# Optimization experiments

Hardware: AMD Instinct MI355X
Metric: run time of the kernel (lower is better)

Reference implementation:

```python
import jax, jax.numpy as jnp
import numpy as np

N = 65536          # total nodes
E = 131072         # total edges
G = 4096           # number of graphs (sessions)
NODES_PER_GRAPH = 16
H = 128            # hidden_dim
D = 64             # embedding_dim
NUM_ITEMS = 50000
NUM_CAT, NUM_SUB, NUM_EL, NUM_BR = 1000, 5000, 10000, 2000
NUM_ITERATIONS = 1


def setup_inputs() -> dict:
    key = jax.random.key(0)
    ks = jax.random.split(key, 24)
    inp = {
        "category": jax.random.randint(ks[0], (N,), 0, NUM_CAT),
        "sub_category": jax.random.randint(ks[1], (N,), 0, NUM_SUB),
        "element": jax.random.randint(ks[2], (N,), 0, NUM_EL),
        "brand": jax.random.randint(ks[3], (N,), 0, NUM_BR),
        "product_id": jax.random.randint(ks[4], (N,), 0, NUM_ITEMS),
        "price": jax.random.uniform(ks[5], (N, 1), dtype=jnp.float32),
        "edge_index": jax.random.randint(ks[6], (2, E), 0, N),
        "batch": jnp.arange(N) // NODES_PER_GRAPH,  # sorted node->graph ids
    }
    s = 0.05
    IN = 5 * D + 1  # 321
    inp["emb_cat"] = jax.random.normal(ks[7], (NUM_CAT, D), jnp.float32) * s
    inp["emb_sub"] = jax.random.normal(ks[8], (NUM_SUB, D), jnp.float32) * s
    inp["emb_el"] = jax.random.normal(ks[9], (NUM_EL, D), jnp.float32) * s
    inp["emb_br"] = jax.random.normal(ks[10], (NUM_BR, D), jnp.float32) * s
    inp["emb_item"] = jax.random.normal(ks[11], (NUM_ITEMS, D), jnp.float32) * s
    inp["Wm"] = jax.random.normal(ks[12], (H, IN), jnp.float32) * s
    inp["bm"] = jnp.zeros((H,), jnp.float32)
    inp["W_ih"] = jax.random.normal(ks[13], (3 * H, H), jnp.float32) * s
    inp["b_ih"] = jnp.zeros((3 * H,), jnp.float32)
    inp["W_hh"] = jax.random.normal(ks[14], (3 * H, H), jnp.float32) * s
    inp["b_hh"] = jnp.zeros((3 * H,), jnp.float32)
    inp["Wg1"] = jax.random.normal(ks[15], (H, H), jnp.float32) * s
    inp["bg1"] = jnp.zeros((H,), jnp.float32)
    inp["Wg2"] = jax.random.normal(ks[16], (1, H), jnp.float32) * s
    inp["bg2"] = jnp.zeros((1,), jnp.float32)
    inp["Wfc"] = jax.random.normal(ks[17], (NUM_ITEMS, H), jnp.float32) * s
    inp["bfc"] = jnp.zeros((NUM_ITEMS,), jnp.float32)
    return inp


def _forward(category, sub_category, element, brand, product_id, price,
             edge_index, batch, emb_cat, emb_sub, emb_el, emb_br, emb_item,
             Wm, bm, W_ih, b_ih, W_hh, b_hh, Wg1, bg1, Wg2, bg2, Wfc, bfc):
    # NodeEmbedding: concat of 5 lookups, then prepend price -> (N, 5D+1)
    emb = jnp.concatenate([
        emb_cat[category], emb_sub[sub_category], emb_el[element],
        emb_br[brand], emb_item[product_id]], axis=1)
    x = jnp.concatenate([price, emb], axis=1)

    # message_linear
    h = x @ Wm.T + bm  # (N, H)

    src, dst = edge_index[0], edge_index[1]  # source -> target
    for _ in range(NUM_ITERATIONS):
        # scatter-mean aggregation of source node embeddings at targets
        msg_sum = jax.ops.segment_sum(h[src], dst, num_segments=N)
        cnt = jax.ops.segment_sum(jnp.ones((E,), h.dtype), dst, num_segments=N)
        m = msg_sum / jnp.maximum(cnt, 1.0)[:, None]
        # GRUCell(m, h), PyTorch gate layout [r, z, n]
        gi = m @ W_ih.T + b_ih
        gh = h @ W_hh.T + b_hh
        gi_r, gi_z, gi_n = jnp.split(gi, 3, axis=1)
        gh_r, gh_z, gh_n = jnp.split(gh, 3, axis=1)
        r = jax.nn.sigmoid(gi_r + gh_r)
        z = jax.nn.sigmoid(gi_z + gh_z)
        n = jnp.tanh(gi_n + r * gh_n)
        h = (1.0 - z) * n + z * h

    # attentional aggregation: segment softmax over batch
    gate = (jax.nn.relu(h @ Wg1.T + bg1) @ Wg2.T + bg2)[:, 0]  # (N,)
    seg_max = jax.ops.segment_max(gate, batch, num_segments=G)
    alpha = jnp.exp(gate - seg_max[batch])
    denom = jax.ops.segment_sum(alpha, batch, num_segments=G)
    w = alpha / denom[batch]
    pooled = jax.ops.segment_sum(w[:, None] * h, batch, num_segments=G)  # (G, H)

    return pooled @ Wfc.T + bfc  # (G, num_items)


def reference(category, sub_category, element, brand, product_id, price,
              edge_index, batch, emb_cat, emb_sub, emb_el, emb_br, emb_item,
              Wm, bm, W_ih, b_ih, W_hh, b_hh, Wg1, bg1, Wg2, bg2, Wfc, bfc):
    return _forward(category, sub_category, element, brand, product_id, price,
                    edge_index, batch, emb_cat, emb_sub, emb_el, emb_br, emb_item,
                    Wm, bm, W_ih, b_ih, W_hh, b_hh, Wg1, bg1, Wg2, bg2, Wfc, bfc)
```

## Files before the change

### kernel.cpp

```cpp
#include <hip/hip_runtime.h>
#include <hip/hip_bf16.h>
#include <cstdint>
#include <cstddef>

#define NN 65536
#define EE 131072
#define GG 4096
#define HH 128
#define DD 64
#define KP 384
#define ITEMS 50000
#define NPAD 50176

typedef __attribute__((ext_vector_type(8))) short bf16x8;
typedef __attribute__((ext_vector_type(4))) float f32x4;
typedef unsigned short u16;
typedef __attribute__((ext_vector_type(4))) unsigned short u16x4;

#define PINV(x) asm volatile("" : "+v"(x))

__device__ inline void split2(float x, u16* hi, u16* lo) {
    __hip_bfloat16 h = __float2bfloat16(x);
    float hf = __bfloat162float(h);
    __hip_bfloat16 l = __float2bfloat16(x - hf);
    *hi = *reinterpret_cast<u16*>(&h);
    *lo = *reinterpret_cast<u16*>(&l);
}
__device__ inline u16 hi_only(float x) {
    __hip_bfloat16 h = __float2bfloat16(x);
    return *reinterpret_cast<u16*>(&h);
}
__device__ inline float bf2f(u16 v) {
    unsigned int u = ((unsigned int)v) << 16;
    return *reinterpret_cast<float*>(&u);
}

__global__ void k_embed(const int* __restrict__ cat, const int* __restrict__ sub,
                        const int* __restrict__ el, const int* __restrict__ br,
                        const int* __restrict__ pid, const float* __restrict__ price,
                        const float* __restrict__ ecat, const float* __restrict__ esub,
                        const float* __restrict__ eel, const float* __restrict__ ebr,
                        const float* __restrict__ eitem, u16* __restrict__ Xhi) {
    int tid = threadIdx.x;
    int n = blockIdx.x * 4 + (tid >> 6);
    int l = tid & 63;
    u16* xh = Xhi + (size_t)n * KP;
    if (l == 0) xh[0] = hi_only(price[n]);
    xh[1 + l]   = hi_only(ecat[(size_t)cat[n] * DD + l]);
    xh[65 + l]  = hi_only(esub[(size_t)sub[n] * DD + l]);
    xh[129 + l] = hi_only(eel [(size_t)el[n]  * DD + l]);
    xh[193 + l] = hi_only(ebr [(size_t)br[n]  * DD + l]);
    xh[257 + l] = hi_only(eitem[(size_t)pid[n]* DD + l]);
    if (l < 63) xh[321 + l] = 0;
}

__global__ void k_cvt_hi(const float* __restrict__ src, u16* __restrict__ hi,
                         int n_valid, int n_total) {
    int i = blockIdx.x * 256 + threadIdx.x;
    if (i >= n_total) return;
    hi[i] = (i < n_valid) ? hi_only(src[i]) : (u16)0;
}

__global__ void k_cvt_wm(const float* __restrict__ Wm, u16* __restrict__ hi) {
    int i = blockIdx.x * 256 + threadIdx.x;
    int r = i / KP, c = i - r * KP;
    float x = (c < 321) ? Wm[r * 321 + c] : 0.f;
    hi[i] = hi_only(x);
}

#define M1_STR 132
__launch_bounds__(256, 2)
__global__ void k_mlp1(const u16* __restrict__ Xhi, const u16* __restrict__ Whi,
                       const float* __restrict__ bm,
                       u16* __restrict__ hhi, u16* __restrict__ hlo) {
    __shared__ float ls[128 * M1_STR];
    int tid = threadIdx.x, w = tid >> 6, l = tid & 63;
    int lr = l & 15, lk = l >> 4;
    int m0 = blockIdx.x * 128;
    f32x4 acc[2][8];
    #pragma unroll
    for (int rt = 0; rt < 2; ++rt)
        #pragma unroll
        for (int ci = 0; ci < 8; ++ci) acc[rt][ci] = (f32x4){0.f, 0.f, 0.f, 0.f};

    for (int kc = 0; kc < 12; ++kc) {
        bf16x8 ah[2];
        #pragma unroll
        for (int rt = 0; rt < 2; ++rt) {
            size_t off = (size_t)(m0 + w * 32 + rt * 16 + lr) * KP + kc * 32 + lk * 8;
            ah[rt] = *(const bf16x8*)(Xhi + off);
        }
        #pragma unroll
        for (int ci = 0; ci < 8; ++ci) {
            size_t boff = (size_t)(ci * 16 + lr) * KP + kc * 32 + lk * 8;
            bf16x8 bh = *(const bf16x8*)(Whi + boff);
            #pragma unroll
            for (int rt = 0; rt < 2; ++rt)
                acc[rt][ci] = __builtin_amdgcn_mfma_f32_16x16x32_bf16(ah[rt], bh, acc[rt][ci], 0, 0, 0);
        }
    }
    #pragma unroll
    for (int rt = 0; rt < 2; ++rt)
        #pragma unroll
        for (int ci = 0; ci < 8; ++ci) {
            int col = ci * 16 + lr;
            float bv = bm[col];
            #pragma unroll
            for (int q = 0; q < 4; ++q)
                ls[(w * 32 + rt * 16 + lk * 4 + q) * M1_STR + col] = acc[rt][ci][q] + bv;
        }
    __syncthreads();
    int row = tid >> 1, cb = (tid & 1) * 64;
    u16* hh = hhi + (size_t)(m0 + row) * HH + cb;
    u16* hl = hlo + (size_t)(m0 + row) * HH + cb;
    #pragma unroll
    for (int i = 0; i < 64; i += 4) {
        float4 v = *(const float4*)&ls[row * M1_STR + cb + i];
        u16x4 vh, vl;
        split2(v.x, (u16*)&vh + 0, (u16*)&vl + 0);
        split2(v.y, (u16*)&vh + 1, (u16*)&vl + 1);
        split2(v.z, (u16*)&vh + 2, (u16*)&vl + 2);
        split2(v.w, (u16*)&vh + 3, (u16*)&vl + 3);
        *(u16x4*)(hh + i) = vh;
        *(u16x4*)(hl + i) = vl;
    }
}

__global__ void k_scatter(const u16* __restrict__ hhi, const int* __restrict__ edge,
                          float* __restrict__ msg, float* __restrict__ cnt) {
    int j = threadIdx.x & 127;
    int eo = threadIdx.x >> 7;
    int e0 = blockIdx.x * 16;
    #pragma unroll
    for (int it = 0; it < 8; ++it) {
        int e = e0 + it * 2 + eo;
        int s = edge[e];
        int d = edge[EE + e];
        atomicAdd(&msg[(size_t)d * HH + j], bf2f(hhi[(size_t)s * HH + j]));
        if (j == 0) atomicAdd(&cnt[d], 1.0f);
    }
}

#define GRU_STR 136
__launch_bounds__(256, 2)
__global__ void k_gru(const float* __restrict__ msg, const float* __restrict__ cnt,
                      const u16* __restrict__ Wihh, const u16* __restrict__ Whhh,
                      const float* __restrict__ b_ih, const float* __restrict__ b_hh,
                      u16* __restrict__ hhi, u16* __restrict__ hlo) {
    __shared__ float ls[32 * GRU_STR];
    int tid = threadIdx.x, w = tid >> 6, l = tid & 63;
    int lr = l & 15, lk = l >> 4;
    int m0 = blockIdx.x * 32;
    f32x4 acc[6][2][2];
    #pragma unroll
    for (int g = 0; g < 6; ++g)
        #pragma unroll
        for (int ct = 0; ct < 2; ++ct)
            #pragma unroll
            for (int rt = 0; rt < 2; ++rt) acc[g][ct][rt] = (f32x4){0.f, 0.f, 0.f, 0.f};

    float cinv[2];
    const float* mrow[2];
    #pragma unroll
    for (int rt = 0; rt < 2; ++rt) {
        int row = m0 + rt * 16 + lr;
        cinv[rt] = 1.0f / fmaxf(cnt[row], 1.0f);
        mrow[rt] = msg + (size_t)row * HH + lk * 8;
    }

    for (int kc = 0; kc < 4; ++kc) {
        bf16x8 amh[2], ahh[2];
        #pragma unroll
        for (int rt = 0; rt < 2; ++rt) {
            float4 v0 = *(const float4*)(mrow[rt] + kc * 32);
            float4 v1 = *(const float4*)(mrow[rt] + kc * 32 + 4);
            float xs[8] = {v0.x * cinv[rt], v0.y * cinv[rt], v0.z * cinv[rt], v0.w * cinv[rt],
                           v1.x * cinv[rt], v1.y * cinv[rt], v1.z * cinv[rt], v1.w * cinv[rt]};
            #pragma unroll
            for (int q = 0; q < 8; ++q) amh[rt][q] = (short)hi_only(xs[q]);
            size_t off = (size_t)(m0 + rt * 16 + lr) * HH + kc * 32 + lk * 8;
            ahh[rt] = *(const bf16x8*)(hhi + off);
        }
        #pragma unroll
        for (int g = 0; g < 6; ++g) {
            const u16* WH = (g < 3) ? Wihh : Whhh;
            int gb = (g % 3) * HH;
            #pragma unroll
            for (int ct = 0; ct < 2; ++ct) {
                size_t boff = (size_t)(gb + w * 32 + ct * 16 + lr) * HH + kc * 32 + lk * 8;
                bf16x8 bh = *(const bf16x8*)(WH + boff);
                #pragma unroll
                for (int rt = 0; rt < 2; ++rt) {
                    bf16x8 ah = (g < 3) ? amh[rt] : ahh[rt];
                    acc[g][ct][rt] = __builtin_amdgcn_mfma_f32_16x16x32_bf16(ah, bh, acc[g][ct][rt], 0, 0, 0);
                }
            }
        }
    }
    #pragma unroll
    for (int ct = 0; ct < 2; ++ct) {
        int col = w * 32 + ct * 16 + lr;
        float bir = b_ih[col], biz = b_ih[HH + col], bin = b_ih[2 * HH + col];
        float bhr = b_hh[col], bhz = b_hh[HH + col], bhn = b_hh[2 * HH + col];
        #pragma unroll
        for (int rt = 0; rt < 2; ++rt)
            #pragma unroll
            for (int q = 0; q < 4; ++q) {
                int rl = rt * 16 + lk * 4 + q;
                size_t idx = (size_t)(m0 + rl) * HH + col;
                float gir = acc[0][ct][rt][q] + bir;
                float giz = acc[1][ct][rt][q] + biz;
                float gin = acc[2][ct][rt][q] + bin;
                float ghr = acc[3][ct][rt][q] + bhr;
                float ghz = acc[4][ct][rt][q] + bhz;
                float ghn = acc[5][ct][rt][q] + bhn;
                float hv = bf2f(hhi[idx]) + bf2f(hlo[idx]);
                float r = 1.f / (1.f + expf(-(gir + ghr)));
                float z = 1.f / (1.f + expf(-(giz + ghz)));
                float nn = tanhf(gin + r * ghn);
                ls[rl * GRU_STR + col] = (1.f - z) * nn + z * hv;
            }
    }
    __syncthreads();
    int row = tid >> 3, cb = (tid & 7) * 16;
    u16* hh = hhi + (size_t)(m0 + row) * HH + cb;
    u16* hl = hlo + (size_t)(m0 + row) * HH + cb;
    #pragma unroll
    for (int i = 0; i < 16; i += 4) {
        float4 v = *(const float4*)&ls[row * GRU_STR + cb + i];
        u16x4 vh, vl;
        split2(v.x, (u16*)&vh + 0, (u16*)&vl + 0);
        split2(v.y, (u16*)&vh + 1, (u16*)&vl + 1);
        split2(v.z, (u16*)&vh + 2, (u16*)&vl + 2);
        split2(v.w, (u16*)&vh + 3, (u16*)&vl + 3);
        *(u16x4*)(hh + i) = vh;
        *(u16x4*)(hl + i) = vl;
    }
}

__launch_bounds__(256, 2)
__global__ void k_gatepool(const u16* __restrict__ hhi, const u16* __restrict__ hlo,
                           const u16* __restrict__ Ghi, const float* __restrict__ bg1,
                           const float* __restrict__ Wg2,
                           u16* __restrict__ phi, u16* __restrict__ plo) {
    __shared__ float sal[128];
    int tid = threadIdx.x, w = tid >> 6, l = tid & 63;
    int lr = l & 15, lk = l >> 4;
    int m0 = blockIdx.x * 128;
    f32x4 acc[2][8];
    #pragma unroll
    for (int rt = 0; rt < 2; ++rt)
        #pragma unroll
        for (int ci = 0; ci < 8; ++ci) acc[rt][ci] = (f32x4){0.f, 0.f, 0.f, 0.f};

    for (int kc = 0; kc < 4; ++kc) {
        bf16x8 ah[2];
        #pragma unroll
        for (int rt = 0; rt < 2; ++rt) {
            size_t off = (size_t)(m0 + w * 32 + rt * 16 + lr) * HH + kc * 32 + lk * 8;
            ah[rt] = *(const bf16x8*)(hhi + off);
        }
        #pragma unroll
        for (int ci = 0; ci < 8; ++ci) {
            size_t boff = (size_t)(ci * 16 + lr) * HH + kc * 32 + lk * 8;
            bf16x8 bh = *(const bf16x8*)(Ghi + boff);
            #pragma unroll
            for (int rt = 0; rt < 2; ++rt)
                acc[rt][ci] = __builtin_amdgcn_mfma_f32_16x16x32_bf16(ah[rt], bh, acc[rt][ci], 0, 0, 0);
        }
    }
    float part[2][4] = {};
    #pragma unroll
    for (int ci = 0; ci < 8; ++ci) {
        int col = ci * 16 + lr;
        float wv = Wg2[col], bb = bg1[col];
        #pragma unroll
        for (int rt = 0; rt < 2; ++rt)
            #pragma unroll
            for (int q = 0; q < 4; ++q)
                part[rt][q] += fmaxf(acc[rt][ci][q] + bb, 0.f) * wv;
    }
    #pragma unroll
    for (int rt = 0; rt < 2; ++rt)
        #pragma unroll
        for (int q = 0; q < 4; ++q) {
            float v = part[rt][q];
            v += __shfl_xor(v, 1);
            v += __shfl_xor(v, 2);
            v += __shfl_xor(v, 4);
            v += __shfl_xor(v, 8);
            part[rt][q] = v;
        }
    if (lr == 0) {
        #pragma unroll
        for (int rt = 0; rt < 2; ++rt)
            #pragma unroll
            for (int q = 0; q < 4; ++q)
                sal[w * 32 + rt * 16 + lk * 4 + q] = part[rt][q];
    }
    __syncthreads();

    int g2 = tid >> 5;
    int c = (tid & 31) * 4;
    int rb = g2 * 16;
    float gv[16];
    float mx = -1e30f;
    #pragma unroll
    for (int i = 0; i < 16; ++i) { gv[i] = sal[rb + i]; mx = fmaxf(mx, gv[i]); }
    float den = 0.f;
    #pragma unroll
    for (int i = 0; i < 16; ++i) { gv[i] = expf(gv[i] - mx); den += gv[i]; }
    float inv = 1.f / den;
    f32x4 a = (f32x4){0.f, 0.f, 0.f, 0.f};
    #pragma unroll
    for (int i = 0; i < 16; ++i) {
        size_t idx = (size_t)(m0 + rb + i) * HH + c;
        u16x4 xh = *(const u16x4*)(hhi + idx);
        u16x4 xl = *(const u16x4*)(hlo + idx);
        float wgt = gv[i] * inv;
        a[0] += wgt * (bf2f(xh.x) + bf2f(xl.x));
        a[1] += wgt * (bf2f(xh.y) + bf2f(xl.y));
        a[2] += wgt * (bf2f(xh.z) + bf2f(xl.z));
        a[3] += wgt * (bf2f(xh.w) + bf2f(xl.w));
    }
    size_t po = (size_t)(blockIdx.x * 8 + g2) * HH + c;
    u16x4 vh, vl;
    #pragma unroll
    for (int q = 0; q < 4; ++q) split2(a[q], (u16*)&vh + q, (u16*)&vl + q);
    *(u16x4*)(phi + po) = vh;
    *(u16x4*)(plo + po) = vl;
}

#define FC_STR 520
__launch_bounds__(256, 2)
__global__ void k_fc13(const u16* __restrict__ Wfcb,
                       const u16* __restrict__ phi, const u16* __restrict__ plo,
                       const float* __restrict__ bfc, float* __restrict__ out) {
    __shared__ float ls[2][16][FC_STR];
    int wg = blockIdx.x;
    int xcd = wg & 7;
    int r = wg >> 3;
    int strip = (r >> 2) * 8 + xcd;
    int phase = r & 3;
    if (strip >= 98) return;
    int tid = threadIdx.x, w = tid >> 6, l = tid & 63;
    int lr = l & 15, lk = l >> 4;
    int c0 = strip * 512;
    int mbase = phase * 1024;

    bf16x8 bh[8][4];
    float bias[8];
    #pragma unroll
    for (int ci = 0; ci < 8; ++ci) {
        int n = c0 + w * 128 + ci * 16 + lr;
        const u16* Wr = Wfcb + (size_t)n * HH + lk * 8;
        #pragma unroll
        for (int kc = 0; kc < 4; ++kc)
            bh[ci][kc] = *(const bf16x8*)(Wr + kc * 32);
        bias[ci] = (n < ITEMS) ? bfc[n] : 0.f;
    }
    #pragma unroll
    for (int ci = 0; ci < 8; ++ci)
        #pragma unroll
        for (int kc = 0; kc < 4; ++kc) PINV(bh[ci][kc]);

    bf16x8 a0h[4], a0l[4], a1h[4], a1l[4];
    auto LOADA = [&](int t, bf16x8* Ah, bf16x8* Al) {
        int m0 = mbase + t * 16;
        size_t aoff = (size_t)(m0 + lr) * HH + lk * 8;
        #pragma unroll
        for (int kc = 0; kc < 4; ++kc) {
            Ah[kc] = *(const bf16x8*)(phi + aoff + kc * 32);
            Al[kc] = *(const bf16x8*)(plo + aoff + kc * 32);
        }
    };
    auto COMP = [&](const bf16x8* Ah, const bf16x8* Al, int b) {
        #pragma unroll
        for (int ci = 0; ci < 8; ++ci) {
            f32x4 acc = (f32x4){0.f, 0.f, 0.f, 0.f};
            #pragma unroll
            for (int kc = 0; kc < 4; ++kc) {
                acc = __builtin_amdgcn_mfma_f32_16x16x32_bf16(Ah[kc], bh[ci][kc], acc, 0, 0, 0);
                acc = __builtin_amdgcn_mfma_f32_16x16x32_bf16(Al[kc], bh[ci][kc], acc, 0, 0, 0);
            }
            #pragma unroll
            for (int q = 0; q < 4; ++q)
                ls[b][lk * 4 + q][w * 128 + ci * 16 + lr] = acc[q] + bias[ci];
        }
    };
    auto FLUSH = [&](int t, int b) {
        int m0 = mbase + t * 16;
        #pragma unroll
        for (int p = 0; p < 4; ++p) {
            int row = w * 4 + p;
            #pragma unroll
            for (int s = 0; s < 2; ++s) {
                int c = s * 256 + l * 4;
                int gc = c0 + c;
                if (gc < ITEMS) {
                    f32x4 v = *(const f32x4*)&ls[b][row][c];
                    __builtin_nontemporal_store(v, (f32x4*)&out[(size_t)(m0 + row) * ITEMS + gc]);
                }
            }
        }
    };
    auto softbar = [&]() {
        asm volatile("s_waitcnt lgkmcnt(0)" ::: "memory");
        __builtin_amdgcn_s_barrier();
    };

    LOADA(0, a0h, a0l);
    LOADA(1, a1h, a1l);
    COMP(a0h, a0l, 0);
    softbar();
    for (int t = 1; t < 64; ++t) {
        if (t + 1 < 64) {
            if ((t + 1) & 1) LOADA(t + 1, a1h, a1l);
            else             LOADA(t + 1, a0h, a0l);
        }
        if (t & 1) COMP(a1h, a1l, 1);
        else       COMP(a0h, a0l, 0);
        FLUSH(t - 1, (t - 1) & 1);
        softbar();
    }
    FLUSH(63, 1);
}

extern "C" void kernel_launch(void* const* d_in, const int* in_sizes, int n_in,
                              void* d_out, int out_size, void* d_ws, size_t ws_size,
                              hipStream_t stream) {
    const int* category = (const int*)d_in[0];
    const int* sub_cat  = (const int*)d_in[1];
    const int* element  = (const int*)d_in[2];
    const int* brand    = (const int*)d_in[3];
    const int* pid      = (const int*)d_in[4];
    const float* price  = (const float*)d_in[5];
    const int* edge     = (const int*)d_in[6];
    const float* ecat   = (const float*)d_in[8];
    const float* esub   = (const float*)d_in[9];
    const float* eel    = (const float*)d_in[10];
    const float* ebr    = (const float*)d_in[11];
    const float* eitem  = (const float*)d_in[12];
    const float* Wm     = (const float*)d_in[13];
    const float* bm     = (const float*)d_in[14];
    const float* W_ih   = (const float*)d_in[15];
    const float* b_ih   = (const float*)d_in[16];
    const float* W_hh   = (const float*)d_in[17];
    const float* b_hh   = (const float*)d_in[18];
    const float* Wg1    = (const float*)d_in[19];
    const float* bg1    = (const float*)d_in[20];
    const float* Wg2    = (const float*)d_in[21];
    const float* Wfc    = (const float*)d_in[23];
    const float* bfc    = (const float*)d_in[24];
    float* out = (float*)d_out;

    char* p = (char*)d_ws;
    auto alloc = [&](size_t bytes) { char* r = p; p += (bytes + 255) & ~(size_t)255; return r; };
    u16* Xhi   = (u16*)alloc((size_t)NN * KP * 2);
    u16* hhi   = (u16*)alloc((size_t)NN * HH * 2);
    u16* hlo   = (u16*)alloc((size_t)NN * HH * 2);
    float* msg = (float*)alloc((size_t)NN * HH * 4);
    float* cnt = (float*)alloc((size_t)NN * 4);
    u16* phi   = (u16*)alloc((size_t)GG * HH * 2);
    u16* plo   = (u16*)alloc((size_t)GG * HH * 2);
    u16* Wmhi  = (u16*)alloc((size_t)HH * KP * 2);
    u16* Wihhi = (u16*)alloc((size_t)3 * HH * HH * 2);
    u16* Whhhi = (u16*)alloc((size_t)3 * HH * HH * 2);
    u16* Wg1hi = (u16*)alloc((size_t)HH * HH * 2);
    u16* Wfcb  = (u16*)alloc((size_t)NPAD * HH * 2);

    hipMemsetAsync(msg, 0, (size_t)NN * HH * sizeof(float), stream);
    hipMemsetAsync(cnt, 0, (size_t)NN * sizeof(float), stream);

    k_cvt_wm<<<(HH * KP + 255) / 256, 256, 0, stream>>>(Wm, Wmhi);
    k_cvt_hi<<<(3 * HH * HH + 255) / 256, 256, 0, stream>>>(W_ih, Wihhi, 3 * HH * HH, 3 * HH * HH);
    k_cvt_hi<<<(3 * HH * HH + 255) / 256, 256, 0, stream>>>(W_hh, Whhhi, 3 * HH * HH, 3 * HH * HH);
    k_cvt_hi<<<(HH * HH + 255) / 256, 256, 0, stream>>>(Wg1, Wg1hi, HH * HH, HH * HH);
    k_cvt_hi<<<(NPAD * HH + 255) / 256, 256, 0, stream>>>(Wfc, Wfcb, ITEMS * HH, NPAD * HH);

    k_embed<<<NN / 4, 256, 0, stream>>>(category, sub_cat, element, brand, pid, price,
                                        ecat, esub, eel, ebr, eitem, Xhi);
    k_mlp1<<<NN / 128, 256, 0, stream>>>(Xhi, Wmhi, bm, hhi, hlo);
    k_scatter<<<EE / 16, 256, 0, stream>>>(hhi, edge, msg, cnt);
    k_gru<<<NN / 32, 256, 0, stream>>>(msg, cnt, Wihhi, Whhhi, b_ih, b_hh, hhi, hlo);
    k_gatepool<<<NN / 128, 256, 0, stream>>>(hhi, hlo, Wg1hi, bg1, Wg2, phi, plo);
    k_fc13<<<dim3(416), 256, 0, stream>>>(Wfcb, phi, plo, bfc, out);
}
```

Before: 423.5 us.

## Accumulate messages in bf16 with packed atomics and fuse prep kernels

Replaces the fp32 message buffer with a bf16 buffer updated via packed bf16 global atomic adds, halving atomic operations and memory traffic in the scatter and GRU read. Also merges embedding gather, buffer zeroing and all weight conversions into a single prep kernel to remove launch and memset overhead. Risks accuracy loss from bf16 accumulation of summed messages.

```diff
diff --git a/kernel.cpp b/kernel.cpp
--- a/kernel.cpp
+++ b/kernel.cpp
@@ -34,38 +34,76 @@
     unsigned int u = ((unsigned int)v) << 16;
     return *reinterpret_cast<float*>(&u);
 }
-
-__global__ void k_embed(const int* __restrict__ cat, const int* __restrict__ sub,
-                        const int* __restrict__ el, const int* __restrict__ br,
-                        const int* __restrict__ pid, const float* __restrict__ price,
-                        const float* __restrict__ ecat, const float* __restrict__ esub,
-                        const float* __restrict__ eel, const float* __restrict__ ebr,
-                        const float* __restrict__ eitem, u16* __restrict__ Xhi) {
+__device__ inline void atomic_pk_bf16(u16* addr, unsigned int data) {
+    asm volatile("global_atomic_pk_add_bf16 %0, %1, off"
+                 :: "v"(addr), "v"(data) : "memory");
+}
+
+#define PREP_EMBED 16384
+#define PREP_MSGZ  4096
+#define PREP_CNTZ  64
+#define PREP_WM    192
+#define PREP_WIH   192
+#define PREP_WHH   192
+#define PREP_WG1   64
+#define PREP_WFC   25088
+__global__ void k_prep(const int* __restrict__ cat, const int* __restrict__ sub,
+                       const int* __restrict__ el, const int* __restrict__ br,
+                       const int* __restrict__ pid, const float* __restrict__ price,
+                       const float* __restrict__ ecat, const float* __restrict__ esub,
+                       const float* __restrict__ eel, const float* __restrict__ ebr,
+                       const float* __restrict__ eitem,
+                       const float* __restrict__ Wm, const float* __restrict__ W_ih,
+                       const float* __restrict__ W_hh, const float* __restrict__ Wg1,
+                       const float* __restrict__ Wfc,
+                       u16* __restrict__ Xhi, u16* __restrict__ msgb,
+                       float* __restrict__ cnt,
+                       u16* __restrict__ Wmhi, u16* __restrict__ Wihhi,
+                       u16* __restrict__ Whhhi, u16* __restrict__ Wg1hi,
+                       u16* __restrict__ Wfcb) {
+    int b = blockIdx.x;
     int tid = threadIdx.x;
-    int n = blockIdx.x * 4 + (tid >> 6);
-    int l = tid & 63;
-    u16* xh = Xhi + (size_t)n * KP;
-    if (l == 0) xh[0] = hi_only(price[n]);
-    xh[1 + l]   = hi_only(ecat[(size_t)cat[n] * DD + l]);
-    xh[65 + l]  = hi_only(esub[(size_t)sub[n] * DD + l]);
-    xh[129 + l] = hi_only(eel [(size_t)el[n]  * DD + l]);
-    xh[193 + l] = hi_only(ebr [(size_t)br[n]  * DD + l]);
-    xh[257 + l] = hi_only(eitem[(size_t)pid[n]* DD + l]);
-    if (l < 63) xh[321 + l] = 0;
-}
-
-__global__ void k_cvt_hi(const float* __restrict__ src, u16* __restrict__ hi,
-                         int n_valid, int n_total) {
-    int i = blockIdx.x * 256 + threadIdx.x;
-    if (i >= n_total) return;
-    hi[i] = (i < n_valid) ? hi_only(src[i]) : (u16)0;
-}
-
-__global__ void k_cvt_wm(const float* __restrict__ Wm, u16* __restrict__ hi) {
-    int i = blockIdx.x * 256 + threadIdx.x;
-    int r = i / KP, c = i - r * KP;
-    float x = (c < 321) ? Wm[r * 321 + c] : 0.f;
-    hi[i] = hi_only(x);
+    if (b < PREP_EMBED) {
+        int n = b * 4 + (tid >> 6);
+        int l = tid & 63;
+        u16* xh = Xhi + (size_t)n * KP;
+        if (l == 0) xh[0] = hi_only(price[n]);
+        xh[1 + l]   = hi_only(ecat[(size_t)cat[n] * DD + l]);
+        xh[65 + l]  = hi_only(esub[(size_t)sub[n] * DD + l]);
+        xh[129 + l] = hi_only(eel [(size_t)el[n]  * DD + l]);
+        xh[193 + l] = hi_only(ebr [(size_t)br[n]  * DD + l]);
+        xh[257 + l] = hi_only(eitem[(size_t)pid[n]* DD + l]);
+        if (l < 63) xh[321 + l] = 0;
+        return;
+    }
+    b -= PREP_EMBED;
+    if (b < PREP_MSGZ) {
+        ((f32x4*)msgb)[(size_t)b * 256 + tid] = (f32x4){0.f, 0.f, 0.f, 0.f};
+        return;
+    }
+    b -= PREP_MSGZ;
+    if (b < PREP_CNTZ) {
+        ((f32x4*)cnt)[(size_t)b * 256 + tid] = (f32x4){0.f, 0.f, 0.f, 0.f};
+        return;
+    }
+    b -= PREP_CNTZ;
+    if (b < PREP_WM) {
+        int i = b * 256 + tid;
+        int r = i / KP, c = i - r * KP;
+        Wmhi[i] = (c < 321) ? hi_only(Wm[r * 321 + c]) : (u16)0;
+        return;
+    }
+    b -= PREP_WM;
+    if (b < PREP_WIH) { int i = b * 256 + tid; Wihhi[i] = hi_only(W_ih[i]); return; }
+    b -= PREP_WIH;
+    if (b < PREP_WHH) { int i = b * 256 + tid; Whhhi[i] = hi_only(W_hh[i]); return; }
+    b -= PREP_WHH;
+    if (b < PREP_WG1) { int i = b * 256 + tid; Wg1hi[i] = hi_only(Wg1[i]); return; }
+    b -= PREP_WG1;
+    {
+        int i = b * 256 + tid;
+        Wfcb[i] = (i < ITEMS * HH) ? hi_only(Wfc[i]) : (u16)0;
+    }
 }
 
 #define M1_STR 132
@@ -127,23 +165,24 @@
 }
 
 __global__ void k_scatter(const u16* __restrict__ hhi, const int* __restrict__ edge,
-                          float* __restrict__ msg, float* __restrict__ cnt) {
-    int j = threadIdx.x & 127;
-    int eo = threadIdx.x >> 7;
+                          u16* __restrict__ msgb, float* __restrict__ cnt) {
+    int w = threadIdx.x >> 6;
+    int l = threadIdx.x & 63;
     int e0 = blockIdx.x * 16;
     #pragma unroll
-    for (int it = 0; it < 8; ++it) {
-        int e = e0 + it * 2 + eo;
+    for (int it = 0; it < 4; ++it) {
+        int e = e0 + it * 4 + w;
         int s = edge[e];
         int d = edge[EE + e];
-        atomicAdd(&msg[(size_t)d * HH + j], bf2f(hhi[(size_t)s * HH + j]));
-        if (j == 0) atomicAdd(&cnt[d], 1.0f);
+        unsigned int pk = *(const unsigned int*)(hhi + (size_t)s * HH + 2 * l);
+        atomic_pk_bf16(msgb + (size_t)d * HH + 2 * l, pk);
+        if (l == 0) atomicAdd(&cnt[d], 1.0f);
     }
 }
 
 #define GRU_STR 136
 __launch_bounds__(256, 2)
-__global__ void k_gru(const float* __restrict__ msg, const float* __restrict__ cnt,
+__global__ void k_gru(const u16* __restrict__ msgb, const float* __restrict__ cnt,
                       const u16* __restrict__ Wihh, const u16* __restrict__ Whhh,
                       const float* __restrict__ b_ih, const float* __restrict__ b_hh,
                       u16* __restrict__ hhi, u16* __restrict__ hlo) {
@@ -160,24 +199,22 @@
             for (int rt = 0; rt < 2; ++rt) acc[g][ct][rt] = (f32x4){0.f, 0.f, 0.f, 0.f};
 
     float cinv[2];
-    const float* mrow[2];
+    const u16* mrowb[2];
     #pragma unroll
     for (int rt = 0; rt < 2; ++rt) {
         int row = m0 + rt * 16 + lr;
         cinv[rt] = 1.0f / fmaxf(cnt[row], 1.0f);
-        mrow[rt] = msg + (size_t)row * HH + lk * 8;
+        mrowb[rt] = msgb + (size_t)row * HH + lk * 8;
     }
 
     for (int kc = 0; kc < 4; ++kc) {
         bf16x8 amh[2], ahh[2];
         #pragma unroll
         for (int rt = 0; rt < 2; ++rt) {
-            float4 v0 = *(const float4*)(mrow[rt] + kc * 32);
-            float4 v1 = *(const float4*)(mrow[rt] + kc * 32 + 4);
-            float xs[8] = {v0.x * cinv[rt], v0.y * cinv[rt], v0.z * cinv[rt], v0.w * cinv[rt],
-                           v1.x * cinv[rt], v1.y * cinv[rt], v1.z * cinv[rt], v1.w * cinv[rt]};
-            #pragma unroll
-            for (int q = 0; q < 8; ++q) amh[rt][q] = (short)hi_only(xs[q]);
+            bf16x8 mv = *(const bf16x8*)(mrowb[rt] + kc * 32);
+            #pragma unroll
+            for (int q = 0; q < 8; ++q)
+                amh[rt][q] = (short)hi_only(bf2f((u16)mv[q]) * cinv[rt]);
             size_t off = (size_t)(m0 + rt * 16 + lr) * HH + kc * 32 + lk * 8;
             ahh[rt] = *(const bf16x8*)(hhi + off);
         }
@@ -459,7 +496,7 @@
     u16* Xhi   = (u16*)alloc((size_t)NN * KP * 2);
     u16* hhi   = (u16*)alloc((size_t)NN * HH * 2);
     u16* hlo   = (u16*)alloc((size_t)NN * HH * 2);
-    float* msg = (float*)alloc((size_t)NN * HH * 4);
+    u16* msgb  = (u16*)alloc((size_t)NN * HH * 2);
     float* cnt = (float*)alloc((size_t)NN * 4);
     u16* phi   = (u16*)alloc((size_t)GG * HH * 2);
     u16* plo   = (u16*)alloc((size_t)GG * HH * 2);
@@ -469,20 +506,16 @@
     u16* Wg1hi = (u16*)alloc((size_t)HH * HH * 2);
     u16* Wfcb  = (u16*)alloc((size_t)NPAD * HH * 2);
 
-    hipMemsetAsync(msg, 0, (size_t)NN * HH * sizeof(float), stream);
-    hipMemsetAsync(cnt, 0, (size_t)NN * sizeof(float), stream);
-
-    k_cvt_wm<<<(HH * KP + 255) / 256, 256, 0, stream>>>(Wm, Wmhi);
-    k_cvt_hi<<<(3 * HH * HH + 255) / 256, 256, 0, stream>>>(W_ih, Wihhi, 3 * HH * HH, 3 * HH * HH);
-    k_cvt_hi<<<(3 * HH * HH + 255) / 256, 256, 0, stream>>>(W_hh, Whhhi, 3 * HH * HH, 3 * HH * HH);
-    k_cvt_hi<<<(HH * HH + 255) / 256, 256, 0, stream>>>(Wg1, Wg1hi, HH * HH, HH * HH);
-    k_cvt_hi<<<(NPAD * HH + 255) / 256, 256, 0, stream>>>(Wfc, Wfcb, ITEMS * HH, NPAD * HH);
-
-    k_embed<<<NN / 4, 256, 0, stream>>>(category, sub_cat, element, brand, pid, price,
-                                        ecat, esub, eel, ebr, eitem, Xhi);
+    const int prep_grid = PREP_EMBED + PREP_MSGZ + PREP_CNTZ + PREP_WM +
+                          PREP_WIH + PREP_WHH + PREP_WG1 + PREP_WFC;
+    k_prep<<<prep_grid, 256, 0, stream>>>(category, sub_cat, element, brand, pid, price,
+                                          ecat, esub, eel, ebr, eitem,
+                                          Wm, W_ih, W_hh, Wg1, Wfc,
+                                          Xhi, msgb, cnt,
+                                          Wmhi, Wihhi, Whhhi, Wg1hi, Wfcb);
     k_mlp1<<<NN / 128, 256, 0, stream>>>(Xhi, Wmhi, bm, hhi, hlo);
-    k_scatter<<<EE / 16, 256, 0, stream>>>(hhi, edge, msg, cnt);
-    k_gru<<<NN / 32, 256, 0, stream>>>(msg, cnt, Wihhi, Whhhi, b_ih, b_hh, hhi, hlo);
+    k_scatter<<<EE / 16, 256, 0, stream>>>(hhi, edge, msgb, cnt);
+    k_gru<<<NN / 32, 256, 0, stream>>>(msgb, cnt, Wihhi, Whhhi, b_ih, b_hh, hhi, hlo);
     k_gatepool<<<NN / 128, 256, 0, stream>>>(hhi, hlo, Wg1hi, bg1, Wg2, phi, plo);
     k_fc13<<<dim3(416), 256, 0, stream>>>(Wfcb, phi, plo, bfc, out);
 }
```

New measurement: 371.7 us. -12.2%, faster.
